# Kernel tuning notes

Measured on AMD Instinct MI355X. Metric: run time of the kernel, lower is better.

## Reference

```python
import jax, jax.numpy as jnp
import numpy as np

B, S, D_IN, E = 64, 199, 1024, 256
INNER, K = 512, 4
NH_M, DH_M = 4, 128
NH_S, DH_S = 4, 64
FF_UP = 384
SLSTM_AT = (1, 4)


def layernorm(x, w, eps=1e-5):
    mu = x.mean(-1, keepdims=True)
    var = x.var(-1, keepdims=True)
    return (x - mu) * jax.lax.rsqrt(var + eps) * w


def mh_layernorm(h, w, eps=1e-5):
    # h: (B,S,NH,DH): normalize per head over DH, scale by w (NH*DH,)
    mu = h.mean(-1, keepdims=True)
    var = h.var(-1, keepdims=True)
    hn = (h - mu) * jax.lax.rsqrt(var + eps)
    b, s, nh, dh = h.shape
    return hn.reshape(b, s, nh * dh) * w


def causal_conv(x, w, b):
    # depthwise causal conv; x (B,S,C), w (C,K), b (C,)
    k = w.shape[-1]
    s = x.shape[1]
    xp = jnp.pad(x, ((0, 0), (k - 1, 0), (0, 0)))
    y = sum(xp[:, i:i + s, :] * w[:, i] for i in range(k))
    return y + b


def headwise(x, w):
    # block-diagonal linear (LinearHeadwiseExpand): x (B,S,H*d), w (H,o,d)
    b, s, _ = x.shape
    h, o, d = w.shape
    y = jnp.einsum('bshd,hod->bsho', x.reshape(b, s, h, d), w)
    return y.reshape(b, s, h * o)


def mlstm_parallel(q, k, v, ig, fg):
    # stabilized parallel mLSTM; q,k,v (B,NH,S,DH); ig,fg (B,NH,S)
    s, dh = q.shape[2], q.shape[3]
    logf = jax.nn.log_sigmoid(fg)
    lfc = jnp.cumsum(logf, axis=-1)
    lfc = jnp.concatenate([jnp.zeros_like(lfc[..., :1]), lfc], axis=-1)  # (B,NH,S+1)
    mat = lfc[..., :, None] - lfc[..., None, :]
    mask = jnp.tril(jnp.ones((s + 1, s + 1), dtype=bool))
    mat = jnp.where(mask, mat, -jnp.inf)
    logD = mat[..., 1:, 1:] + ig[..., None, :]            # (B,NH,S,S)
    maxD = jnp.max(logD, axis=-1, keepdims=True)
    Dm = jnp.exp(logD - maxD)
    qk = jnp.einsum('bnsd,bntd->bnst', q, k) / (dh ** 0.5)
    C = qk * Dm
    norm = jnp.maximum(jnp.abs(C.sum(-1, keepdims=True)), jnp.exp(-maxD))
    return jnp.einsum('bnst,bntd->bnsd', C / (norm + 1e-6), v)


def mlstm_layer(x, proj_up, conv_w, conv_b, q_w, k_w, v_w, ig_w, ig_b, fg_w, fg_b, skip, outnorm_w, proj_down):
    b, s, _ = x.shape
    xi = x @ proj_up                                      # (B,S,2*INNER)
    x_m, z = jnp.split(xi, 2, axis=-1)
    xca = jax.nn.silu(causal_conv(x_m, conv_w, conv_b))
    q = headwise(xca, q_w)
    k = headwise(xca, k_w)
    v = headwise(x_m, v_w)
    gate_in = jnp.concatenate([q, k, v], axis=-1)         # (B,S,3*INNER)
    ig = (gate_in @ ig_w.T + ig_b).transpose(0, 2, 1)     # (B,NH,S)
    fg = (gate_in @ fg_w.T + fg_b).transpose(0, 2, 1)
    qh = q.reshape(b, s, NH_M, DH_M).transpose(0, 2, 1, 3)
    kh = k.reshape(b, s, NH_M, DH_M).transpose(0, 2, 1, 3)
    vh = v.reshape(b, s, NH_M, DH_M).transpose(0, 2, 1, 3)
    h = mlstm_parallel(qh, kh, vh, ig, fg)                # (B,NH,S,DH)
    hn = mh_layernorm(h.transpose(0, 2, 1, 3), outnorm_w) # (B,S,INNER)
    h_state = (hn + skip * xca) * jax.nn.silu(z)
    return h_state @ proj_down


def slstm_layer(x, conv_w, conv_b, gate_w, rec_w, bias, gn_w):
    b, s, _ = x.shape
    xc = jax.nn.silu(causal_conv(x, conv_w, conv_b))
    xch = xc.reshape(b, s, NH_S, DH_S)
    xh = x.reshape(b, s, NH_S, DH_S)
    gi = jnp.einsum('bshd,hod->bsho', xch, gate_w[0])
    gf = jnp.einsum('bshd,hod->bsho', xch, gate_w[1])
    gz = jnp.einsum('bshd,hod->bsho', xh, gate_w[2])
    go = jnp.einsum('bshd,hod->bsho', xh, gate_w[3])
    Wx = jnp.stack([gi, gf, gz, go], axis=2)              # (B,S,4,NH,DH)

    def step(carry, wx):
        h, c, n, m = carry
        raw = wx + jnp.einsum('bhd,ghod->bgho', h, rec_w) + bias
        iraw, fraw, zraw, oraw = raw[:, 0], raw[:, 1], raw[:, 2], raw[:, 3]
        logfplusm = m + jax.nn.log_sigmoid(fraw)
        m_new = jnp.maximum(iraw, logfplusm)
        igate = jnp.exp(iraw - m_new)
        fgate = jnp.exp(logfplusm - m_new)
        c_new = fgate * c + igate * jnp.tanh(zraw)
        n_new = fgate * n + igate
        h_new = jax.nn.sigmoid(oraw) * (c_new / n_new)
        return (h_new, c_new, n_new, m_new), h_new

    z0 = jnp.zeros((b, NH_S, DH_S), x.dtype)
    _, ys = jax.lax.scan(step, (z0, z0, z0, z0), jnp.moveaxis(Wx, 1, 0))
    y = jnp.moveaxis(ys, 0, 1)                            # (B,S,NH,DH)
    return mh_layernorm(y, gn_w)


def gated_ffn(x, w_up, w_dn):
    gate, up = jnp.split(x @ w_up, 2, axis=-1)
    return (jax.nn.gelu(gate) * up) @ w_dn


def forward_fn(x, w_down, b_down, m_ln_w, m_proj_up, m_conv_w, m_conv_b, m_q_w, m_k_w, m_v_w,
               m_ig_w, m_ig_b, m_fg_w, m_fg_b, m_skip, m_outnorm_w, m_proj_down,
               s_ln_w, s_conv_w, s_conv_b, s_gate_w, s_rec_w, s_bias, s_gn_w, s_ln2_w,
               s_ffn_up, s_ffn_down, post_ln_w, w_emo, b_emo, w_sen, b_sen):
    h = x @ w_down + b_down                               # (B,S,E)
    mi = si = 0
    for blk in range(7):
        if blk in SLSTM_AT:
            h = h + slstm_layer(layernorm(h, s_ln_w[si]), s_conv_w[si], s_conv_b[si],
                                s_gate_w[si], s_rec_w[si], s_bias[si], s_gn_w[si])
            h = h + gated_ffn(layernorm(h, s_ln2_w[si]), s_ffn_up[si], s_ffn_down[si])
            si += 1
        else:
            h = h + mlstm_layer(layernorm(h, m_ln_w[mi]), m_proj_up[mi], m_conv_w[mi], m_conv_b[mi],
                                m_q_w[mi], m_k_w[mi], m_v_w[mi], m_ig_w[mi], m_ig_b[mi],
                                m_fg_w[mi], m_fg_b[mi], m_skip[mi], m_outnorm_w[mi], m_proj_down[mi])
            mi += 1
    h = jax.nn.selu(layernorm(h, post_ln_w))
    pooled = h.mean(axis=1)                               # (B,E)
    return pooled @ w_emo + b_emo, pooled @ w_sen + b_sen


def setup_inputs() -> dict:
    ks = iter(jax.random.split(jax.random.key(0), 40))
    def p(*shape, s=0.02):
        return jax.random.normal(next(ks), shape, dtype=jnp.float32) * s
    inp = dict(
        x=jax.random.normal(next(ks), (B, S, D_IN), dtype=jnp.float32),
        w_down=p(D_IN, E), b_down=jnp.zeros((E,), jnp.float32),
        m_ln_w=jnp.ones((5, E), jnp.float32),
        m_proj_up=p(5, E, 2 * INNER),
        m_conv_w=p(5, INNER, K), m_conv_b=jnp.zeros((5, INNER), jnp.float32),
        m_q_w=p(5, 128, 4, 4), m_k_w=p(5, 128, 4, 4), m_v_w=p(5, 128, 4, 4),
        m_ig_w=p(5, NH_M, 3 * INNER), m_ig_b=p(5, NH_M, s=0.1),
        m_fg_w=p(5, NH_M, 3 * INNER),
        m_fg_b=jnp.tile(jnp.linspace(3.0, 6.0, NH_M, dtype=jnp.float32), (5, 1)),
        m_skip=jnp.ones((5, INNER), jnp.float32),
        m_outnorm_w=jnp.ones((5, INNER), jnp.float32),
        m_proj_down=p(5, INNER, E),
        s_ln_w=jnp.ones((2, E), jnp.float32),
        s_conv_w=p(2, E, K), s_conv_b=jnp.zeros((2, E), jnp.float32),
        s_gate_w=p(2, 4, NH_S, DH_S, DH_S),
        s_rec_w=p(2, 4, NH_S, DH_S, DH_S),
        s_bias=jnp.zeros((2, 4, NH_S, DH_S), jnp.float32).at[:, 1].set(3.0),
        s_gn_w=jnp.ones((2, E), jnp.float32),
        s_ln2_w=jnp.ones((2, E), jnp.float32),
        s_ffn_up=p(2, E, 2 * FF_UP), s_ffn_down=p(2, FF_UP, E),
        post_ln_w=jnp.ones((E,), jnp.float32),
        w_emo=p(E, 7), b_emo=jnp.zeros((7,), jnp.float32),
        w_sen=p(E, 3), b_sen=jnp.zeros((3,), jnp.float32),
    )
    return inp


def reference(x, w_down, b_down, m_ln_w, m_proj_up, m_conv_w, m_conv_b, m_q_w, m_k_w, m_v_w,
              m_ig_w, m_ig_b, m_fg_w, m_fg_b, m_skip, m_outnorm_w, m_proj_down,
              s_ln_w, s_conv_w, s_conv_b, s_gate_w, s_rec_w, s_bias, s_gn_w, s_ln2_w,
              s_ffn_up, s_ffn_down, post_ln_w, w_emo, b_emo, w_sen, b_sen):
    return forward_fn(x, w_down, b_down, m_ln_w, m_proj_up, m_conv_w, m_conv_b, m_q_w, m_k_w, m_v_w,
                      m_ig_w, m_ig_b, m_fg_w, m_fg_b, m_skip, m_outnorm_w, m_proj_down,
                      s_ln_w, s_conv_w, s_conv_b, s_gate_w, s_rec_w, s_bias, s_gn_w, s_ln2_w,
                      s_ffn_up, s_ffn_down, post_ln_w, w_emo, b_emo, w_sen, b_sen)
```

## Files before the change

### kernel.cpp

```cpp
#include <hip/hip_runtime.h>
#include <hip/hip_bf16.h>
#include <math.h>


#define B_    64
#define S_    199
#define E_    256
#define NTOK  (B_*S_)
#define NQT   13

typedef __attribute__((ext_vector_type(8))) short short8;
typedef __attribute__((ext_vector_type(4))) float floatx4;
typedef unsigned short ushort_t;

__device__ __forceinline__ float sigmoidf_(float x) { return 1.f / (1.f + expf(-x)); }
__device__ __forceinline__ float siluf_(float x) { return x / (1.f + expf(-x)); }
__device__ __forceinline__ float logsigf_(float x) { return fminf(x, 0.f) - log1pf(expf(-fabsf(x))); }

__device__ __forceinline__ ushort_t f2b(float f) {
    union { float f; unsigned u; } v; v.f = f;
    unsigned r = (v.u + 0x7fffu + ((v.u >> 16) & 1u)) >> 16;
    return (ushort_t)r;
}
__device__ __forceinline__ float bf2f(ushort_t u) {
    union { unsigned u; float f; } v; v.u = ((unsigned)u) << 16;
    return v.f;
}
__device__ __forceinline__ short8 cvt8(const float* p) {
    union { ushort_t us[8]; short8 v; } t;
    #pragma unroll
    for (int i = 0; i < 8; i++) t.us[i] = f2b(p[i]);
    return t.v;
}

__global__ void cvt_bf(const float* __restrict__ in, ushort_t* __restrict__ out, int n4) {
    int i = blockIdx.x * 256 + threadIdx.x;
    if (i >= n4) return;
    float4 v = *(const float4*)&in[i * 4];
    union { ushort_t us[4]; uint2 u; } t;
    t.us[0] = f2b(v.x); t.us[1] = f2b(v.y); t.us[2] = f2b(v.z); t.us[3] = f2b(v.w);
    *(uint2*)&out[i * 4] = t.u;
}

__global__ void __launch_bounds__(256)
gemm_bf(const ushort_t* __restrict__ A, const ushort_t* __restrict__ Bw,
        const float* __restrict__ bias, float* __restrict__ C,
        int M, int K, int N, int accum) {
    __shared__ __align__(16) ushort_t As[64][40];
    __shared__ __align__(16) ushort_t Bs[128][40];
    int tid = threadIdx.x;
    int wave = tid >> 6, lane = tid & 63;
    int wm = wave >> 1, wn = wave & 1;
    int quad = lane >> 4, l16 = lane & 15;
    int m0 = blockIdx.y * 64, n0 = blockIdx.x * 128;
    floatx4 zero = {0.f, 0.f, 0.f, 0.f};
    floatx4 acc[2][4];
    #pragma unroll
    for (int i = 0; i < 2; i++)
        #pragma unroll
        for (int j = 0; j < 4; j++) acc[i][j] = zero;
    int ar = tid >> 2, ac = (tid & 3) * 8;
    int bn = tid & 127, bkg = (tid >> 7) * 16;
    for (int k0 = 0; k0 < K; k0 += 32) {
        *(uint4*)&As[ar][ac] = *(const uint4*)(A + (size_t)(m0 + ar) * K + k0 + ac);
        {
            const ushort_t* bp = Bw + (size_t)(k0 + bkg) * N + n0 + bn;
            union { ushort_t us[16]; uint4 v[2]; } t;
            #pragma unroll
            for (int i = 0; i < 16; i++) t.us[i] = bp[(size_t)i * N];
            *(uint4*)&Bs[bn][bkg] = t.v[0];
            *(uint4*)&Bs[bn][bkg + 8] = t.v[1];
        }
        __syncthreads();
        short8 af[2], bf[4];
        #pragma unroll
        for (int i = 0; i < 2; i++) af[i] = *(const short8*)&As[wm * 32 + i * 16 + l16][quad * 8];
        #pragma unroll
        for (int j = 0; j < 4; j++) bf[j] = *(const short8*)&Bs[wn * 64 + j * 16 + l16][quad * 8];
        #pragma unroll
        for (int i = 0; i < 2; i++)
            #pragma unroll
            for (int j = 0; j < 4; j++)
                acc[i][j] = __builtin_amdgcn_mfma_f32_16x16x32_bf16(af[i], bf[j], acc[i][j], 0, 0, 0);
        __syncthreads();
    }
    #pragma unroll
    for (int i = 0; i < 2; i++)
        #pragma unroll
        for (int j = 0; j < 4; j++)
            #pragma unroll
            for (int r = 0; r < 4; r++) {
                int row = m0 + wm * 32 + i * 16 + quad * 4 + r;
                int col = n0 + wn * 64 + j * 16 + l16;
                float o = acc[i][j][r];
                if (bias) o += bias[col];
                float* cp = &C[(size_t)row * N + col];
                if (accum) o += *cp;
                *cp = o;
            }
}

__global__ void __launch_bounds__(256)
gemm_mfma(const float* __restrict__ A, const float* __restrict__ Bw,
          const float* __restrict__ bias, float* __restrict__ C,
          int M, int K, int N, int accum) {
    __shared__ __align__(16) ushort_t As[64][40];
    __shared__ __align__(16) ushort_t Bs[64][40];
    int tid = threadIdx.x;
    int wave = tid >> 6, lane = tid & 63;
    int wm = wave >> 1, wn = wave & 1;
    int quad = lane >> 4, l16 = lane & 15;
    int m0 = blockIdx.y * 64, n0 = blockIdx.x * 64;
    floatx4 zero = {0.f, 0.f, 0.f, 0.f};
    floatx4 acc[2][2];
    acc[0][0] = zero; acc[0][1] = zero; acc[1][0] = zero; acc[1][1] = zero;
    int ar = tid >> 2, ac = (tid & 3) * 8;
    int bn = tid & 63, bk = (tid >> 6) * 8;
    for (int k0 = 0; k0 < K; k0 += 32) {
        {
            const float* ap = A + (size_t)(m0 + ar) * K + k0 + ac;
            union { ushort_t us[8]; uint4 v; } t;
            #pragma unroll
            for (int i = 0; i < 8; i++) t.us[i] = f2b(ap[i]);
            *(uint4*)&As[ar][ac] = t.v;
        }
        {
            const float* bp = Bw + (size_t)(k0 + bk) * N + n0 + bn;
            union { ushort_t us[8]; uint4 v; } t;
            #pragma unroll
            for (int i = 0; i < 8; i++) t.us[i] = f2b(bp[(size_t)i * N]);
            *(uint4*)&Bs[bn][bk] = t.v;
        }
        __syncthreads();
        short8 af[2], bf[2];
        #pragma unroll
        for (int i = 0; i < 2; i++) af[i] = *(const short8*)&As[wm * 32 + i * 16 + l16][quad * 8];
        #pragma unroll
        for (int j = 0; j < 2; j++) bf[j] = *(const short8*)&Bs[wn * 32 + j * 16 + l16][quad * 8];
        #pragma unroll
        for (int i = 0; i < 2; i++)
            #pragma unroll
            for (int j = 0; j < 2; j++)
                acc[i][j] = __builtin_amdgcn_mfma_f32_16x16x32_bf16(af[i], bf[j], acc[i][j], 0, 0, 0);
        __syncthreads();
    }
    #pragma unroll
    for (int i = 0; i < 2; i++)
        #pragma unroll
        for (int j = 0; j < 2; j++)
            #pragma unroll
            for (int r = 0; r < 4; r++) {
                int row = m0 + wm * 32 + i * 16 + quad * 4 + r;
                int col = n0 + wn * 32 + j * 16 + l16;
                float o = acc[i][j][r];
                if (bias) o += bias[col];
                float* cp = &C[(size_t)row * N + col];
                if (accum) o += *cp;
                *cp = o;
            }
}

__global__ void __launch_bounds__(256)
slstm_wx_mfma(const ushort_t* __restrict__ xc, const ushort_t* __restrict__ xln,
              const float* __restrict__ gw, float* __restrict__ Wx) {
    __shared__ __align__(16) ushort_t As[64][40];
    __shared__ __align__(16) ushort_t Bs[64][40];
    int gh = blockIdx.y; int g = gh >> 2, hh = gh & 3;
    const ushort_t* src = (g < 2) ? xc : xln;
    const float* w = gw + (size_t)gh * 4096;
    int tid = threadIdx.x;
    int wave = tid >> 6, lane = tid & 63;
    int wm = wave >> 1, wn = wave & 1;
    int quad = lane >> 4, l16 = lane & 15;
    int m0 = blockIdx.x * 64;
    floatx4 zero = {0.f, 0.f, 0.f, 0.f};
    floatx4 acc[2][2];
    acc[0][0] = zero; acc[0][1] = zero; acc[1][0] = zero; acc[1][1] = zero;
    int ar = tid >> 2, ac = (tid & 3) * 8;
    int bn = tid & 63, bk = (tid >> 6) * 8;
    #pragma unroll
    for (int kt = 0; kt < 2; kt++) {
        int k0 = kt * 32;
        *(uint4*)&As[ar][ac] = *(const uint4*)(src + (size_t)(m0 + ar) * 256 + hh * 64 + k0 + ac);
        {
            const float* bp = w + (size_t)bn * 64 + k0 + bk;
            union { ushort_t us[8]; uint4 v; } t;
            #pragma unroll
            for (int i = 0; i < 8; i++) t.us[i] = f2b(bp[i]);
            *(uint4*)&Bs[bn][bk] = t.v;
        }
        __syncthreads();
        short8 af[2], bf[2];
        #pragma unroll
        for (int i = 0; i < 2; i++) af[i] = *(const short8*)&As[wm * 32 + i * 16 + l16][quad * 8];
        #pragma unroll
        for (int j = 0; j < 2; j++) bf[j] = *(const short8*)&Bs[wn * 32 + j * 16 + l16][quad * 8];
        #pragma unroll
        for (int i = 0; i < 2; i++)
            #pragma unroll
            for (int j = 0; j < 2; j++)
                acc[i][j] = __builtin_amdgcn_mfma_f32_16x16x32_bf16(af[i], bf[j], acc[i][j], 0, 0, 0);
        __syncthreads();
    }
    #pragma unroll
    for (int i = 0; i < 2; i++)
        #pragma unroll
        for (int j = 0; j < 2; j++)
            #pragma unroll
            for (int r = 0; r < 4; r++) {
                int row = m0 + wm * 32 + i * 16 + quad * 4 + r;
                int col = wn * 32 + j * 16 + l16;
                Wx[(size_t)row * 1024 + g * 256 + hh * 64 + col] = acc[i][j][r];
            }
}

__global__ void __launch_bounds__(256)
layernorm256(const float* __restrict__ x, const float* __restrict__ w, ushort_t* __restrict__ y) {
    int n = blockIdx.x, t = threadIdx.x;
    float v = x[(size_t)n * 256 + t];
    float s = v, s2 = v * v;
    #pragma unroll
    for (int off = 32; off; off >>= 1) { s += __shfl_xor(s, off); s2 += __shfl_xor(s2, off); }
    __shared__ float ps[4], ps2[4];
    if ((t & 63) == 0) { ps[t >> 6] = s; ps2[t >> 6] = s2; }
    __syncthreads();
    float S = ps[0] + ps[1] + ps[2] + ps[3];
    float S2 = ps2[0] + ps2[1] + ps2[2] + ps2[3];
    float mu = S / 256.f, var = S2 / 256.f - mu * mu;
    y[(size_t)n * 256 + t] = f2b((v - mu) * rsqrtf(var + 1e-5f) * w[t]);
}

__global__ void __launch_bounds__(256)
postln_selu(const float* __restrict__ x, const float* __restrict__ w, float* __restrict__ y) {
    int n = blockIdx.x, t = threadIdx.x;
    float v = x[(size_t)n * 256 + t];
    float s = v, s2 = v * v;
    #pragma unroll
    for (int off = 32; off; off >>= 1) { s += __shfl_xor(s, off); s2 += __shfl_xor(s2, off); }
    __shared__ float ps[4], ps2[4];
    if ((t & 63) == 0) { ps[t >> 6] = s; ps2[t >> 6] = s2; }
    __syncthreads();
    float S = ps[0] + ps[1] + ps[2] + ps[3];
    float S2 = ps2[0] + ps2[1] + ps2[2] + ps2[3];
    float mu = S / 256.f, var = S2 / 256.f - mu * mu;
    float yn = (v - mu) * rsqrtf(var + 1e-5f) * w[t];
    y[(size_t)n * 256 + t] = 1.0507009873554805f * (yn > 0.f ? yn : 1.6732632423543772f * (expf(yn) - 1.f));
}

__global__ void conv_silu_m(const float* __restrict__ xi, const float* __restrict__ cw,
                            const float* __restrict__ cb, float* __restrict__ xca) {
    int idx = blockIdx.x * blockDim.x + threadIdx.x;
    if (idx >= NTOK * 512) return;
    int n = idx >> 9, c = idx & 511;
    int b = n / S_, s = n - b * S_;
    float y = cb[c];
    #pragma unroll
    for (int i = 0; i < 4; i++) {
        int sp = s - 3 + i;
        if (sp >= 0) y += xi[(size_t)(b * S_ + sp) * 1024 + c] * cw[c * 4 + i];
    }
    xca[idx] = siluf_(y);
}

__global__ void headwise_qkv(const float* __restrict__ xca, const float* __restrict__ xi,
                             const float* __restrict__ qw, const float* __restrict__ kw,
                             const float* __restrict__ vw,
                             float* __restrict__ qb, float* __restrict__ kb, float* __restrict__ vb) {
    int idx = blockIdx.x * blockDim.x + threadIdx.x;
    if (idx >= NTOK * 512) return;
    int n = idx >> 9, c = idx & 511;
    int hh = c >> 2, o = c & 3;
    float aq = 0, ak = 0, av = 0;
    #pragma unroll
    for (int d = 0; d < 4; d++) {
        float xc = xca[(size_t)n * 512 + hh * 4 + d];
        float xm = xi[(size_t)n * 1024 + hh * 4 + d];
        int wi = (hh * 4 + o) * 4 + d;
        aq += xc * qw[wi]; ak += xc * kw[wi]; av += xm * vw[wi];
    }
    qb[idx] = aq; kb[idx] = ak; vb[idx] = av;
}

__global__ void __launch_bounds__(256)
mlstm_gates(const float* __restrict__ qb, const float* __restrict__ kb, const float* __restrict__ vb,
            const float* __restrict__ igw, const float* __restrict__ igbias,
            const float* __restrict__ fgw, const float* __restrict__ fgbias,
            float* __restrict__ igo, float* __restrict__ fgo) {
    int gid = blockIdx.x * 256 + threadIdx.x;
    int wid = gid >> 6, lane = gid & 63;
    int which = wid & 1, hd = (wid >> 1) & 3, n = wid >> 3;
    if (n >= NTOK) return;
    const float* w = (which ? fgw : igw) + hd * 1536;
    float a = 0.f;
    for (int j = lane; j < 512; j += 64) {
        a += qb[(size_t)n * 512 + j] * w[j]
           + kb[(size_t)n * 512 + j] * w[512 + j]
           + vb[(size_t)n * 512 + j] * w[1024 + j];
    }
    #pragma unroll
    for (int off = 32; off; off >>= 1) a += __shfl_xor(a, off);
    if (lane == 0) {
        a += (which ? fgbias : igbias)[hd];
        (which ? fgo : igo)[(size_t)n * 4 + hd] = a;
    }
}

__global__ void __launch_bounds__(256)
mlstm_cumsum(const float* __restrict__ fgo, const float* __restrict__ igo,
             float* __restrict__ lfc, float* __restrict__ Mx) {
    int bh = blockIdx.x * 4 + (threadIdx.x >> 6);
    int lane = threadIdx.x & 63;
    int b = bh >> 2, h = bh & 3;
    float v[4]; float lsum = 0.f;
    #pragma unroll
    for (int i = 0; i < 4; i++) {
        int s = lane * 4 + i;
        float f = (s < S_) ? fgo[(size_t)(b * S_ + s) * 4 + h] : 0.f;
        lsum += logsigf_(f);
        v[i] = lsum;
    }
    float x = lsum;
    #pragma unroll
    for (int off = 1; off < 64; off <<= 1) {
        float y = __shfl_up(x, off);
        if (lane >= off) x += y;
    }
    float excl = x - lsum;
    float lf1[4];
    #pragma unroll
    for (int i = 0; i < 4; i++) lf1[i] = excl + v[i];
    if (lane == 0) lfc[bh * (S_ + 1)] = 0.f;
    #pragma unroll
    for (int i = 0; i < 4; i++) {
        int s = lane * 4 + i;
        if (s < S_) lfc[bh * (S_ + 1) + s + 1] = lf1[i];
    }
    float gm[4]; float lmax = -1e30f;
    #pragma unroll
    for (int i = 0; i < 4; i++) {
        int s = lane * 4 + i;
        float ig_ = (s < S_) ? igo[(size_t)(b * S_ + s) * 4 + h] : -1e30f;
        float gg = ig_ - lf1[i];
        lmax = fmaxf(lmax, gg);
        gm[i] = lmax;
    }
    float xm = lmax;
    #pragma unroll
    for (int off = 1; off < 64; off <<= 1) {
        float y = __shfl_up(xm, off);
        if (lane >= off) xm = fmaxf(xm, y);
    }
    float exclm = __shfl_up(xm, 1);
    if (lane == 0) exclm = -1e30f;
    #pragma unroll
    for (int i = 0; i < 4; i++) {
        int s = lane * 4 + i;
        if (s < S_) Mx[bh * S_ + s] = fmaxf(exclm, gm[i]);
    }
}

__global__ void __launch_bounds__(256, 1)
mlstm_attn_mfma(const float* __restrict__ qb, const float* __restrict__ kb, const float* __restrict__ vb,
                const float* __restrict__ igb, const float* __restrict__ lfc, const float* __restrict__ Mx,
                float* __restrict__ outb) {
    __shared__ __align__(16) ushort_t Kb[64 * 136];
    __shared__ __align__(16) ushort_t Vt[128 * 72];
    __shared__ __align__(16) ushort_t Pw[4][16 * 72];
    __shared__ float gv[208], lfv[208], mxv[208];
    int bh = blockIdx.x; int b = bh >> 2, h = bh & 3;
    int tid = threadIdx.x, wave = tid >> 6, lane = tid & 63;
    int quad = lane >> 4, l16 = lane & 15;
    if (tid < 208) {
        if (tid < S_) {
            float lf1 = lfc[bh * (S_ + 1) + tid + 1];
            gv[tid] = igb[(size_t)(b * S_ + tid) * 4 + h] - lf1;
            lfv[tid] = lf1;
            mxv[tid] = Mx[bh * S_ + tid];
        } else { gv[tid] = 0.f; lfv[tid] = 0.f; mxv[tid] = 0.f; }
    }
    floatx4 zero = {0.f, 0.f, 0.f, 0.f};
    float rs[4][4];
    floatx4 accv[4][8];
    #pragma unroll
    for (int qi = 0; qi < 4; qi++) {
        #pragma unroll
        for (int r = 0; r < 4; r++) rs[qi][r] = 0.f;
        #pragma unroll
        for (int dt = 0; dt < 8; dt++) accv[qi][dt] = zero;
    }
    const float scale = 0.08838834764831845f;
    int trow = tid >> 4, d0 = (tid & 15) * 8;
    for (int c = 0; c < 4; c++) {
        __syncthreads();
        #pragma unroll
        for (int i = 0; i < 4; i++) {
            int tl = trow + 16 * i;
            int t = c * 64 + tl;
            union { ushort_t us[8]; uint4 v; } kk;
            ushort_t vv[8];
            if (t < S_) {
                const float* kp = kb + (size_t)(b * S_ + t) * 512 + h * 128 + d0;
                const float* vp = vb + (size_t)(b * S_ + t) * 512 + h * 128 + d0;
                #pragma unroll
                for (int ii = 0; ii < 8; ii++) { kk.us[ii] = f2b(kp[ii]); vv[ii] = f2b(vp[ii]); }
            } else {
                kk.v = (uint4){0, 0, 0, 0};
                #pragma unroll
                for (int ii = 0; ii < 8; ii++) vv[ii] = 0;
            }
            *(uint4*)&Kb[tl * 136 + d0] = kk.v;
            #pragma unroll
            for (int ii = 0; ii < 8; ii++) Vt[(d0 + ii) * 72 + tl] = vv[ii];
        }
        __syncthreads();
        for (int qi = 0; qi < 4; qi++) {
            int qt = wave + 4 * qi;
            if (qt >= NQT || qt < 4 * c) continue;
            uint4 z4 = {0, 0, 0, 0};
            for (int z = lane; z < 144; z += 64) ((uint4*)Pw[wave])[z] = z4;
            int srow = qt * 16 + l16;
            const float* qp = qb + (size_t)(b * S_ + min(srow, S_ - 1)) * 512 + h * 128 + quad * 8;
            short8 af[4];
            #pragma unroll
            for (int ks = 0; ks < 4; ks++) af[ks] = cvt8(qp + 32 * ks);
            int ktmax_l = min(qt, 4 * c + 3) - 4 * c;
            for (int ktl = 0; ktl <= ktmax_l; ktl++) {
                floatx4 acc = zero;
                #pragma unroll
                for (int ks = 0; ks < 4; ks++) {
                    short8 bf = *(const short8*)&Kb[(ktl * 16 + l16) * 136 + quad * 8 + 32 * ks];
                    acc = __builtin_amdgcn_mfma_f32_16x16x32_bf16(af[ks], bf, acc, 0, 0, 0);
                }
                int tcol = c * 64 + ktl * 16 + l16;
                float gt = gv[tcol];
                #pragma unroll
                for (int r = 0; r < 4; r++) {
                    int s = qt * 16 + quad * 4 + r;
                    bool valid = (tcol <= s) && (tcol < S_);
                    float w = valid ? expf(gt - mxv[s]) : 0.f;
                    float p = acc[r] * scale * w;
                    rs[qi][r] += p;
                    Pw[wave][(quad * 4 + r) * 72 + ktl * 16 + l16] = f2b(p);
                }
            }
            #pragma unroll
            for (int dt = 0; dt < 8; dt++) {
                floatx4 a = accv[qi][dt];
                #pragma unroll
                for (int ks = 0; ks < 2; ks++) {
                    short8 ap = *(const short8*)&Pw[wave][l16 * 72 + quad * 8 + 32 * ks];
                    short8 bp = *(const short8*)&Vt[(dt * 16 + l16) * 72 + quad * 8 + 32 * ks];
                    a = __builtin_amdgcn_mfma_f32_16x16x32_bf16(ap, bp, a, 0, 0, 0);
                }
                accv[qi][dt] = a;
            }
        }
    }
    for (int qi = 0; qi < 4; qi++) {
        int qt = wave + 4 * qi;
        if (qt >= NQT) continue;
        float nrm[4];
        #pragma unroll
        for (int r = 0; r < 4; r++) {
            float v = rs[qi][r];
            v += __shfl_xor(v, 1); v += __shfl_xor(v, 2);
            v += __shfl_xor(v, 4); v += __shfl_xor(v, 8);
            int s = qt * 16 + quad * 4 + r;
            nrm[r] = fmaxf(fabsf(v), expf(-(lfv[s] + mxv[s]))) + 1e-6f;
        }
        #pragma unroll
        for (int dt = 0; dt < 8; dt++)
            #pragma unroll
            for (int r = 0; r < 4; r++) {
                int s = qt * 16 + quad * 4 + r;
                if (s < S_)
                    outb[(size_t)(b * S_ + s) * 512 + h * 128 + dt * 16 + l16] = accv[qi][dt][r] / nrm[r];
            }
    }
}

__global__ void __launch_bounds__(512)
mhln_m(float* __restrict__ hatt, const float* __restrict__ w) {
    int n = blockIdx.x, t = threadIdx.x;
    float v = hatt[(size_t)n * 512 + t];
    float s = v, s2 = v * v;
    #pragma unroll
    for (int off = 32; off; off >>= 1) { s += __shfl_xor(s, off); s2 += __shfl_xor(s2, off); }
    __shared__ float ps[8], ps2[8];
    if ((t & 63) == 0) { ps[t >> 6] = s; ps2[t >> 6] = s2; }
    __syncthreads();
    int hd = t >> 7;
    float S = ps[hd * 2] + ps[hd * 2 + 1], S2 = ps2[hd * 2] + ps2[hd * 2 + 1];
    float mu = S / 128.f, var = S2 / 128.f - mu * mu;
    hatt[(size_t)n * 512 + t] = (v - mu) * rsqrtf(var + 1e-5f) * w[t];
}

__global__ void hstate_m(const float* __restrict__ hatt, const float* __restrict__ xca,
                         const float* __restrict__ xi, const float* __restrict__ skip,
                         ushort_t* __restrict__ out16) {
    int idx = blockIdx.x * blockDim.x + threadIdx.x;
    if (idx >= NTOK * 512) return;
    int n = idx >> 9, c = idx & 511;
    float z = xi[(size_t)n * 1024 + 512 + c];
    out16[idx] = f2b((hatt[idx] + skip[c] * xca[idx]) * siluf_(z));
}

__global__ void conv_silu_s(const ushort_t* __restrict__ xln, const float* __restrict__ cw,
                            const float* __restrict__ cb, ushort_t* __restrict__ xc) {
    int idx = blockIdx.x * blockDim.x + threadIdx.x;
    if (idx >= NTOK * 256) return;
    int n = idx >> 8, c = idx & 255;
    int b = n / S_, s = n - b * S_;
    float y = cb[c];
    #pragma unroll
    for (int i = 0; i < 4; i++) {
        int sp = s - 3 + i;
        if (sp >= 0) y += bf2f(xln[(size_t)(b * S_ + sp) * 256 + c]) * cw[c * 4 + i];
    }
    xc[idx] = f2b(siluf_(y));
}

__global__ void __launch_bounds__(512)
slstm_rec(const float* __restrict__ Wx, const float* __restrict__ rw,
          const float* __restrict__ bias, float* __restrict__ ys) {
    int b = blockIdx.x >> 2, h = blockIdx.x & 3;
    int tid = threadIdx.x;
    int g = tid >> 7;
    int o = (tid >> 1) & 63;
    int kh = tid & 1;
    float w[32];
    const float* wp = rw + (size_t)(((g * 4 + h) * 64 + o)) * 64 + kh * 32;
    #pragma unroll
    for (int d = 0; d < 32; d++) w[d] = wp[d];
    float bi = bias[(g * 4 + h) * 64 + o];
    __shared__ __align__(16) float hs[64];
    __shared__ float raws[4][64];
    if (tid < 64) hs[tid] = 0.f;
    float c_ = 0.f, n_ = 0.f, m_ = 0.f;
    size_t wxbase = (size_t)(b * S_) * 1024 + g * 256 + h * 64 + o;
    float wx_cur = Wx[wxbase];
    __syncthreads();
    for (int s = 0; s < S_; s++) {
        float wx_next = (s + 1 < S_) ? Wx[wxbase + (size_t)(s + 1) * 1024] : 0.f;
        float a0 = 0.f, a1 = 0.f, a2 = 0.f, a3 = 0.f;
        const float* hb = hs + kh * 32;
        #pragma unroll
        for (int d4 = 0; d4 < 8; d4++) {
            float4 hv = *(const float4*)&hb[d4 * 4];
            a0 += hv.x * w[4 * d4 + 0];
            a1 += hv.y * w[4 * d4 + 1];
            a2 += hv.z * w[4 * d4 + 2];
            a3 += hv.w * w[4 * d4 + 3];
        }
        float a = (a0 + a1) + (a2 + a3);
        a += __shfl_xor(a, 1);
        if (kh == 0) raws[g][o] = a + wx_cur + bi;
        __syncthreads();
        float ir = raws[0][o], fr = raws[1][o], zr = raws[2][o], orr = raws[3][o];
        float lfpm = m_ + logsigf_(fr);
        float mn = fmaxf(ir, lfpm);
        float ig = expf(ir - mn), fg = expf(lfpm - mn);
        c_ = fg * c_ + ig * tanhf(zr);
        n_ = fg * n_ + ig;
        m_ = mn;
        float hn = sigmoidf_(orr) * (c_ / n_);
        if (g == 0 && kh == 0) {
            hs[o] = hn;
            ys[(size_t)(b * S_ + s) * 256 + h * 64 + o] = hn;
        }
        __syncthreads();
        wx_cur = wx_next;
    }
}

__global__ void __launch_bounds__(256)
mhln_s_resid(const float* __restrict__ ys, const float* __restrict__ w, float* __restrict__ h) {
    int n = blockIdx.x, t = threadIdx.x;
    float v = ys[(size_t)n * 256 + t];
    float s = v, s2 = v * v;
    #pragma unroll
    for (int off = 32; off; off >>= 1) { s += __shfl_xor(s, off); s2 += __shfl_xor(s2, off); }
    float mu = s / 64.f, var = s2 / 64.f - mu * mu;
    h[(size_t)n * 256 + t] += (v - mu) * rsqrtf(var + 1e-5f) * w[t];
}

__global__ void ffn_act(const float* __restrict__ up, ushort_t* __restrict__ act) {
    int idx = blockIdx.x * blockDim.x + threadIdx.x;
    if (idx >= NTOK * 384) return;
    int n = idx / 384, j = idx - n * 384;
    float g = up[(size_t)n * 768 + j], u = up[(size_t)n * 768 + 384 + j];
    float t = tanhf(0.7978845608028654f * (g + 0.044715f * g * g * g));
    act[idx] = f2b(0.5f * g * (1.f + t) * u);
}

__global__ void pool_k(const float* __restrict__ a, float* __restrict__ pooled) {
    int b = blockIdx.x, e = threadIdx.x;
    float s = 0.f;
    for (int t = 0; t < S_; t++) s += a[(size_t)(b * S_ + t) * 256 + e];
    pooled[b * 256 + e] = s / (float)S_;
}

__global__ void heads_k(const float* __restrict__ pooled,
                        const float* __restrict__ we, const float* __restrict__ be,
                        const float* __restrict__ ws, const float* __restrict__ bs,
                        float* __restrict__ out) {
    int i = blockIdx.x * blockDim.x + threadIdx.x;
    if (i < B_ * 7) {
        int b = i / 7, o = i - b * 7;
        float a = be[o];
        for (int e = 0; e < 256; e++) a += pooled[b * 256 + e] * we[e * 7 + o];
        out[b * 7 + o] = a;
    } else if (i < B_ * 7 + B_ * 3) {
        int j = i - B_ * 7;
        int b = j / 3, o = j - b * 3;
        float a = bs[o];
        for (int e = 0; e < 256; e++) a += pooled[b * 256 + e] * ws[e * 3 + o];
        out[B_ * 7 + b * 3 + o] = a;
    }
}

extern "C" void kernel_launch(void* const* d_in, const int* in_sizes, int n_in,
                              void* d_out, int out_size, void* d_ws, size_t ws_size,
                              hipStream_t stream) {
    (void)in_sizes; (void)n_in; (void)out_size; (void)ws_size;
    const float* x          = (const float*)d_in[0];
    const float* w_down     = (const float*)d_in[1];
    const float* b_down     = (const float*)d_in[2];
    const float* m_ln_w     = (const float*)d_in[3];
    const float* m_proj_up  = (const float*)d_in[4];
    const float* m_conv_w   = (const float*)d_in[5];
    const float* m_conv_b   = (const float*)d_in[6];
    const float* m_q_w      = (const float*)d_in[7];
    const float* m_k_w      = (const float*)d_in[8];
    const float* m_v_w      = (const float*)d_in[9];
    const float* m_ig_w     = (const float*)d_in[10];
    const float* m_ig_b     = (const float*)d_in[11];
    const float* m_fg_w     = (const float*)d_in[12];
    const float* m_fg_b     = (const float*)d_in[13];
    const float* m_skip     = (const float*)d_in[14];
    const float* m_outnorm  = (const float*)d_in[15];
    const float* m_proj_dn  = (const float*)d_in[16];
    const float* s_ln_w     = (const float*)d_in[17];
    const float* s_conv_w   = (const float*)d_in[18];
    const float* s_conv_b   = (const float*)d_in[19];
    const float* s_gate_w   = (const float*)d_in[20];
    const float* s_rec_w    = (const float*)d_in[21];
    const float* s_bias     = (const float*)d_in[22];
    const float* s_gn_w     = (const float*)d_in[23];
    const float* s_ln2_w    = (const float*)d_in[24];
    const float* s_ffn_up   = (const float*)d_in[25];
    const float* s_ffn_dn   = (const float*)d_in[26];
    const float* post_ln_w  = (const float*)d_in[27];
    const float* w_emo      = (const float*)d_in[28];
    const float* b_emo      = (const float*)d_in[29];
    const float* w_sen      = (const float*)d_in[30];
    const float* b_sen      = (const float*)d_in[31];

    float* W    = (float*)d_ws;
    float* h    = W;
    float* lnb  = h    + (size_t)NTOK * 256;
    float* big0 = lnb  + (size_t)NTOK * 256;
    float* xca  = big0 + (size_t)NTOK * 1024;
    float* qb   = xca  + (size_t)NTOK * 512;
    float* kb   = qb   + (size_t)NTOK * 512;
    float* vb   = kb   + (size_t)NTOK * 512;
    float* hatt = vb   + (size_t)NTOK * 512;
    float* igo  = hatt + (size_t)NTOK * 512;
    float* fgo  = igo  + (size_t)NTOK * 4;
    float* lfcb = fgo  + (size_t)NTOK * 4;
    float* Mxb  = lfcb + (size_t)256 * (S_ + 1);
    float* pooled = Mxb + (size_t)256 * S_;
    ushort_t* lnb16 = (ushort_t*)lnb;
    ushort_t* hat16 = (ushort_t*)kb;
    ushort_t* xc16  = (ushort_t*)vb;
    ushort_t* wpk   = (ushort_t*)(pooled + 64 * 256);
    ushort_t* wp_pu = wpk;
    ushort_t* wp_pd = wp_pu + 5 * 262144;
    ushort_t* wp_fu = wp_pd + 5 * 131072;
    ushort_t* wp_fd = wp_fu + 2 * 196608;

    cvt_bf<<<(5 * 262144 / 4 + 255) / 256, 256, 0, stream>>>(m_proj_up, wp_pu, 5 * 262144 / 4);
    cvt_bf<<<(5 * 131072 / 4 + 255) / 256, 256, 0, stream>>>(m_proj_dn, wp_pd, 5 * 131072 / 4);
    cvt_bf<<<(2 * 196608 / 4 + 255) / 256, 256, 0, stream>>>(s_ffn_up, wp_fu, 2 * 196608 / 4);
    cvt_bf<<<(2 * 98304 / 4 + 255) / 256, 256, 0, stream>>>(s_ffn_dn, wp_fd, 2 * 98304 / 4);

    gemm_mfma<<<dim3(256 / 64, NTOK / 64), 256, 0, stream>>>(x, w_down, b_down, h, NTOK, 1024, 256, 0);

    int mi = 0, si = 0;
    for (int blk = 0; blk < 7; blk++) {
        if (blk == 1 || blk == 4) {
            layernorm256<<<NTOK, 256, 0, stream>>>(h, s_ln_w + si * 256, lnb16);
            conv_silu_s<<<(NTOK * 256 + 255) / 256, 256, 0, stream>>>(lnb16, s_conv_w + si * 1024, s_conv_b + si * 256, xc16);
            slstm_wx_mfma<<<dim3(NTOK / 64, 16), 256, 0, stream>>>(xc16, lnb16, s_gate_w + (size_t)si * 65536, big0);
            slstm_rec<<<256, 512, 0, stream>>>(big0, s_rec_w + (size_t)si * 65536, s_bias + si * 1024, hatt);
            mhln_s_resid<<<NTOK, 256, 0, stream>>>(hatt, s_gn_w + si * 256, h);
            layernorm256<<<NTOK, 256, 0, stream>>>(h, s_ln2_w + si * 256, lnb16);
            gemm_bf<<<dim3(768 / 128, NTOK / 64), 256, 0, stream>>>(lnb16, wp_fu + (size_t)si * 196608, nullptr, big0, NTOK, 256, 768, 0);
            ffn_act<<<(NTOK * 384 + 255) / 256, 256, 0, stream>>>(big0, hat16);
            gemm_bf<<<dim3(256 / 128, NTOK / 64), 256, 0, stream>>>(hat16, wp_fd + (size_t)si * 98304, nullptr, h, NTOK, 384, 256, 1);
            si++;
        } else {
            layernorm256<<<NTOK, 256, 0, stream>>>(h, m_ln_w + mi * 256, lnb16);
            gemm_bf<<<dim3(1024 / 128, NTOK / 64), 256, 0, stream>>>(lnb16, wp_pu + (size_t)mi * 262144, nullptr, big0, NTOK, 256, 1024, 0);
            conv_silu_m<<<(NTOK * 512 + 255) / 256, 256, 0, stream>>>(big0, m_conv_w + mi * 2048, m_conv_b + mi * 512, xca);
            headwise_qkv<<<(NTOK * 512 + 255) / 256, 256, 0, stream>>>(xca, big0, m_q_w + mi * 2048, m_k_w + mi * 2048, m_v_w + mi * 2048, qb, kb, vb);
            mlstm_gates<<<NTOK * 2, 256, 0, stream>>>(qb, kb, vb, m_ig_w + mi * 6144, m_ig_b + mi * 4, m_fg_w + mi * 6144, m_fg_b + mi * 4, igo, fgo);
            mlstm_cumsum<<<64, 256, 0, stream>>>(fgo, igo, lfcb, Mxb);
            mlstm_attn_mfma<<<256, 256, 0, stream>>>(qb, kb, vb, igo, lfcb, Mxb, hatt);
            mhln_m<<<NTOK, 512, 0, stream>>>(hatt, m_outnorm + mi * 512);
            hstate_m<<<(NTOK * 512 + 255) / 256, 256, 0, stream>>>(hatt, xca, big0, m_skip + mi * 512, hat16);
            gemm_bf<<<dim3(256 / 128, NTOK / 64), 256, 0, stream>>>(hat16, wp_pd + (size_t)mi * 131072, nullptr, h, NTOK, 512, 256, 1);
            mi++;
        }
    }

    postln_selu<<<NTOK, 256, 0, stream>>>(h, post_ln_w, xca);
    pool_k<<<B_, 256, 0, stream>>>(xca, pooled);
    heads_k<<<3, 256, 0, stream>>>(pooled, w_emo, b_emo, w_sen, b_sen, (float*)d_out);
}
```

Before: 2.289 ms.

## Fuse mLSTM conv/qkv, store q/k/v in bf16, fuse out-norm with hstate

Merges the causal conv+SiLU and headwise q/k/v projections into one kernel that writes q/k/v as bf16. The gate projection is rewritten to read the bf16 tensors, with one wave per token computing all eight gate dot products. The attention kernel now loads bf16 directly instead of converting fp32 on the fly. The multi-head layernorm is fused with the h-state/skip/gating kernel. The sLSTM recurrent weights move from registers to shared memory. These changes cut launches and global memory traffic, at the cost of bf16 rounding for the gate inputs and extra LDS pressure in the recurrence.

```diff
diff --git a/kernel.cpp b/kernel.cpp
--- a/kernel.cpp
+++ b/kernel.cpp
@@ -26,11 +26,10 @@
     union { unsigned u; float f; } v; v.u = ((unsigned)u) << 16;
     return v.f;
 }
-__device__ __forceinline__ short8 cvt8(const float* p) {
-    union { ushort_t us[8]; short8 v; } t;
-    #pragma unroll
-    for (int i = 0; i < 8; i++) t.us[i] = f2b(p[i]);
-    return t.v;
+__device__ __forceinline__ void unp2(unsigned d, float& lo, float& hi) {
+    union { unsigned u; float f; } a, b;
+    a.u = d << 16; b.u = d & 0xffff0000u;
+    lo = a.f; hi = b.f;
 }
 
 __global__ void cvt_bf(const float* __restrict__ in, ushort_t* __restrict__ out, int n4) {
@@ -247,61 +246,100 @@
     y[(size_t)n * 256 + t] = 1.0507009873554805f * (yn > 0.f ? yn : 1.6732632423543772f * (expf(yn) - 1.f));
 }
 
-__global__ void conv_silu_m(const float* __restrict__ xi, const float* __restrict__ cw,
-                            const float* __restrict__ cb, float* __restrict__ xca) {
-    int idx = blockIdx.x * blockDim.x + threadIdx.x;
-    if (idx >= NTOK * 512) return;
-    int n = idx >> 9, c = idx & 511;
+__global__ void __launch_bounds__(256)
+fused_qkv(const float* __restrict__ xi, const float* __restrict__ cw,
+          const float* __restrict__ cb,
+          const float* __restrict__ qw, const float* __restrict__ kw,
+          const float* __restrict__ vw,
+          float* __restrict__ xca,
+          ushort_t* __restrict__ q16, ushort_t* __restrict__ k16, ushort_t* __restrict__ v16) {
+    int idx = blockIdx.x * 256 + threadIdx.x;
+    if (idx >= NTOK * 128) return;
+    int n = idx >> 7, hh = idx & 127;
     int b = n / S_, s = n - b * S_;
-    float y = cb[c];
+    int c0 = hh * 4;
+    float4 hist[4];
     #pragma unroll
     for (int i = 0; i < 4; i++) {
         int sp = s - 3 + i;
-        if (sp >= 0) y += xi[(size_t)(b * S_ + sp) * 1024 + c] * cw[c * 4 + i];
-    }
-    xca[idx] = siluf_(y);
-}
-
-__global__ void headwise_qkv(const float* __restrict__ xca, const float* __restrict__ xi,
-                             const float* __restrict__ qw, const float* __restrict__ kw,
-                             const float* __restrict__ vw,
-                             float* __restrict__ qb, float* __restrict__ kb, float* __restrict__ vb) {
-    int idx = blockIdx.x * blockDim.x + threadIdx.x;
-    if (idx >= NTOK * 512) return;
-    int n = idx >> 9, c = idx & 511;
-    int hh = c >> 2, o = c & 3;
-    float aq = 0, ak = 0, av = 0;
+        if (sp >= 0) hist[i] = *(const float4*)(xi + (size_t)(b * S_ + sp) * 1024 + c0);
+        else hist[i] = (float4){0.f, 0.f, 0.f, 0.f};
+    }
+    float xm[4] = {hist[3].x, hist[3].y, hist[3].z, hist[3].w};
+    float xc4[4];
     #pragma unroll
     for (int d = 0; d < 4; d++) {
-        float xc = xca[(size_t)n * 512 + hh * 4 + d];
-        float xm = xi[(size_t)n * 1024 + hh * 4 + d];
-        int wi = (hh * 4 + o) * 4 + d;
-        aq += xc * qw[wi]; ak += xc * kw[wi]; av += xm * vw[wi];
-    }
-    qb[idx] = aq; kb[idx] = ak; vb[idx] = av;
-}
-
-__global__ void __launch_bounds__(256)
-mlstm_gates(const float* __restrict__ qb, const float* __restrict__ kb, const float* __restrict__ vb,
-            const float* __restrict__ igw, const float* __restrict__ igbias,
-            const float* __restrict__ fgw, const float* __restrict__ fgbias,
-            float* __restrict__ igo, float* __restrict__ fgo) {
-    int gid = blockIdx.x * 256 + threadIdx.x;
-    int wid = gid >> 6, lane = gid & 63;
-    int which = wid & 1, hd = (wid >> 1) & 3, n = wid >> 3;
-    if (n >= NTOK) return;
-    const float* w = (which ? fgw : igw) + hd * 1536;
-    float a = 0.f;
-    for (int j = lane; j < 512; j += 64) {
-        a += qb[(size_t)n * 512 + j] * w[j]
-           + kb[(size_t)n * 512 + j] * w[512 + j]
-           + vb[(size_t)n * 512 + j] * w[1024 + j];
-    }
-    #pragma unroll
-    for (int off = 32; off; off >>= 1) a += __shfl_xor(a, off);
-    if (lane == 0) {
-        a += (which ? fgbias : igbias)[hd];
-        (which ? fgo : igo)[(size_t)n * 4 + hd] = a;
+        float y = cb[c0 + d];
+        const float* cwp = cw + (c0 + d) * 4;
+        y += hist[0].x * 0.f;
+        float hv[4] = { d==0?hist[0].x:(d==1?hist[0].y:(d==2?hist[0].z:hist[0].w)),
+                        d==0?hist[1].x:(d==1?hist[1].y:(d==2?hist[1].z:hist[1].w)),
+                        d==0?hist[2].x:(d==1?hist[2].y:(d==2?hist[2].z:hist[2].w)),
+                        xm[d] };
+        #pragma unroll
+        for (int i = 0; i < 4; i++) y += hv[i] * cwp[i];
+        xc4[d] = siluf_(y);
+    }
+    *(float4*)(xca + (size_t)n * 512 + c0) = (float4){xc4[0], xc4[1], xc4[2], xc4[3]};
+    union { ushort_t us[4]; uint2 u; } qo, ko, vo;
+    #pragma unroll
+    for (int o = 0; o < 4; o++) {
+        const float* qp = qw + (c0 + o) * 4;
+        const float* kp = kw + (c0 + o) * 4;
+        const float* vp = vw + (c0 + o) * 4;
+        float aq = 0.f, ak = 0.f, av = 0.f;
+        #pragma unroll
+        for (int d = 0; d < 4; d++) {
+            aq += xc4[d] * qp[d];
+            ak += xc4[d] * kp[d];
+            av += xm[d] * vp[d];
+        }
+        qo.us[o] = f2b(aq); ko.us[o] = f2b(ak); vo.us[o] = f2b(av);
+    }
+    *(uint2*)(q16 + (size_t)n * 512 + c0) = qo.u;
+    *(uint2*)(k16 + (size_t)n * 512 + c0) = ko.u;
+    *(uint2*)(v16 + (size_t)n * 512 + c0) = vo.u;
+}
+
+__global__ void __launch_bounds__(256)
+gates2(const ushort_t* __restrict__ qb, const ushort_t* __restrict__ kb, const ushort_t* __restrict__ vb,
+       const float* __restrict__ igw, const float* __restrict__ igbias,
+       const float* __restrict__ fgw, const float* __restrict__ fgbias,
+       float* __restrict__ igo, float* __restrict__ fgo) {
+    int n = blockIdx.x * 4 + (threadIdx.x >> 6);
+    int lane = threadIdx.x & 63;
+    uint4 q4 = *(const uint4*)(qb + (size_t)n * 512 + lane * 8);
+    uint4 k4 = *(const uint4*)(kb + (size_t)n * 512 + lane * 8);
+    uint4 v4 = *(const uint4*)(vb + (size_t)n * 512 + lane * 8);
+    float q[8], k[8], v[8];
+    unp2(q4.x, q[0], q[1]); unp2(q4.y, q[2], q[3]); unp2(q4.z, q[4], q[5]); unp2(q4.w, q[6], q[7]);
+    unp2(k4.x, k[0], k[1]); unp2(k4.y, k[2], k[3]); unp2(k4.z, k[4], k[5]); unp2(k4.w, k[6], k[7]);
+    unp2(v4.x, v[0], v[1]); unp2(v4.y, v[2], v[3]); unp2(v4.z, v[4], v[5]); unp2(v4.w, v[6], v[7]);
+    float acc[8];
+    #pragma unroll
+    for (int hd = 0; hd < 4; hd++)
+        #pragma unroll
+        for (int wh = 0; wh < 2; wh++) {
+            const float* w = (wh ? fgw : igw) + hd * 1536 + lane * 8;
+            float a = 0.f;
+            #pragma unroll
+            for (int i = 0; i < 8; i++) a += q[i] * w[i];
+            #pragma unroll
+            for (int i = 0; i < 8; i++) a += k[i] * w[512 + i];
+            #pragma unroll
+            for (int i = 0; i < 8; i++) a += v[i] * w[1024 + i];
+            acc[hd * 2 + wh] = a;
+        }
+    #pragma unroll
+    for (int t = 0; t < 8; t++) {
+        float a = acc[t];
+        #pragma unroll
+        for (int off = 32; off; off >>= 1) a += __shfl_xor(a, off);
+        if (lane == 0) {
+            int hd = t >> 1, wh = t & 1;
+            a += (wh ? fgbias : igbias)[hd];
+            (wh ? fgo : igo)[(size_t)n * 4 + hd] = a;
+        }
     }
 }
 
@@ -360,7 +398,7 @@
 }
 
 __global__ void __launch_bounds__(256, 1)
-mlstm_attn_mfma(const float* __restrict__ qb, const float* __restrict__ kb, const float* __restrict__ vb,
+mlstm_attn_mfma(const ushort_t* __restrict__ qb, const ushort_t* __restrict__ kb, const ushort_t* __restrict__ vb,
                 const float* __restrict__ igb, const float* __restrict__ lfc, const float* __restrict__ Mx,
                 float* __restrict__ outb) {
     __shared__ __align__(16) ushort_t Kb[64 * 136];
@@ -396,21 +434,17 @@
         for (int i = 0; i < 4; i++) {
             int tl = trow + 16 * i;
             int t = c * 64 + tl;
-            union { ushort_t us[8]; uint4 v; } kk;
-            ushort_t vv[8];
+            union { ushort_t us[8]; uint4 v; } kk, vv;
             if (t < S_) {
-                const float* kp = kb + (size_t)(b * S_ + t) * 512 + h * 128 + d0;
-                const float* vp = vb + (size_t)(b * S_ + t) * 512 + h * 128 + d0;
-                #pragma unroll
-                for (int ii = 0; ii < 8; ii++) { kk.us[ii] = f2b(kp[ii]); vv[ii] = f2b(vp[ii]); }
+                kk.v = *(const uint4*)(kb + (size_t)(b * S_ + t) * 512 + h * 128 + d0);
+                vv.v = *(const uint4*)(vb + (size_t)(b * S_ + t) * 512 + h * 128 + d0);
             } else {
                 kk.v = (uint4){0, 0, 0, 0};
-                #pragma unroll
-                for (int ii = 0; ii < 8; ii++) vv[ii] = 0;
+                vv.v = (uint4){0, 0, 0, 0};
             }
             *(uint4*)&Kb[tl * 136 + d0] = kk.v;
             #pragma unroll
-            for (int ii = 0; ii < 8; ii++) Vt[(d0 + ii) * 72 + tl] = vv[ii];
+            for (int ii = 0; ii < 8; ii++) Vt[(d0 + ii) * 72 + tl] = vv.us[ii];
         }
         __syncthreads();
         for (int qi = 0; qi < 4; qi++) {
@@ -419,10 +453,10 @@
             uint4 z4 = {0, 0, 0, 0};
             for (int z = lane; z < 144; z += 64) ((uint4*)Pw[wave])[z] = z4;
             int srow = qt * 16 + l16;
-            const float* qp = qb + (size_t)(b * S_ + min(srow, S_ - 1)) * 512 + h * 128 + quad * 8;
+            const ushort_t* qp = qb + (size_t)(b * S_ + min(srow, S_ - 1)) * 512 + h * 128 + quad * 8;
             short8 af[4];
             #pragma unroll
-            for (int ks = 0; ks < 4; ks++) af[ks] = cvt8(qp + 32 * ks);
+            for (int ks = 0; ks < 4; ks++) af[ks] = *(const short8*)(qp + 32 * ks);
             int ktmax_l = min(qt, 4 * c + 3) - 4 * c;
             for (int ktl = 0; ktl <= ktmax_l; ktl++) {
                 floatx4 acc = zero;
@@ -480,7 +514,9 @@
 }
 
 __global__ void __launch_bounds__(512)
-mhln_m(float* __restrict__ hatt, const float* __restrict__ w) {
+mhln_hstate(const float* __restrict__ hatt, const float* __restrict__ w,
+            const float* __restrict__ xca, const float* __restrict__ xi,
+            const float* __restrict__ skip, ushort_t* __restrict__ out16) {
     int n = blockIdx.x, t = threadIdx.x;
     float v = hatt[(size_t)n * 512 + t];
     float s = v, s2 = v * v;
@@ -492,17 +528,9 @@
     int hd = t >> 7;
     float S = ps[hd * 2] + ps[hd * 2 + 1], S2 = ps2[hd * 2] + ps2[hd * 2 + 1];
     float mu = S / 128.f, var = S2 / 128.f - mu * mu;
-    hatt[(size_t)n * 512 + t] = (v - mu) * rsqrtf(var + 1e-5f) * w[t];
-}
-
-__global__ void hstate_m(const float* __restrict__ hatt, const float* __restrict__ xca,
-                         const float* __restrict__ xi, const float* __restrict__ skip,
-                         ushort_t* __restrict__ out16) {
-    int idx = blockIdx.x * blockDim.x + threadIdx.x;
-    if (idx >= NTOK * 512) return;
-    int n = idx >> 9, c = idx & 511;
-    float z = xi[(size_t)n * 1024 + 512 + c];
-    out16[idx] = f2b((hatt[idx] + skip[c] * xca[idx]) * siluf_(z));
+    float hn = (v - mu) * rsqrtf(var + 1e-5f) * w[t];
+    float z = xi[(size_t)n * 1024 + 512 + t];
+    out16[(size_t)n * 512 + t] = f2b((hn + skip[t] * xca[(size_t)n * 512 + t]) * siluf_(z));
 }
 
 __global__ void conv_silu_s(const ushort_t* __restrict__ xln, const float* __restrict__ cw,
@@ -523,18 +551,17 @@
 __global__ void __launch_bounds__(512)
 slstm_rec(const float* __restrict__ Wx, const float* __restrict__ rw,
           const float* __restrict__ bias, float* __restrict__ ys) {
+    __shared__ __align__(16) float wl[512 * 36];
+    __shared__ __align__(16) float hs[64];
+    __shared__ float raws[4][64];
     int b = blockIdx.x >> 2, h = blockIdx.x & 3;
     int tid = threadIdx.x;
-    int g = tid >> 7;
-    int o = (tid >> 1) & 63;
-    int kh = tid & 1;
-    float w[32];
+    int g = tid >> 7, o = (tid >> 1) & 63, kh = tid & 1;
     const float* wp = rw + (size_t)(((g * 4 + h) * 64 + o)) * 64 + kh * 32;
-    #pragma unroll
-    for (int d = 0; d < 32; d++) w[d] = wp[d];
+    float* myrow = wl + tid * 36;
+    #pragma unroll
+    for (int i = 0; i < 8; i++) *(float4*)&myrow[i * 4] = *(const float4*)&wp[i * 4];
     float bi = bias[(g * 4 + h) * 64 + o];
-    __shared__ __align__(16) float hs[64];
-    __shared__ float raws[4][64];
     if (tid < 64) hs[tid] = 0.f;
     float c_ = 0.f, n_ = 0.f, m_ = 0.f;
     size_t wxbase = (size_t)(b * S_) * 1024 + g * 256 + h * 64 + o;
@@ -543,14 +570,14 @@
     for (int s = 0; s < S_; s++) {
         float wx_next = (s + 1 < S_) ? Wx[wxbase + (size_t)(s + 1) * 1024] : 0.f;
         float a0 = 0.f, a1 = 0.f, a2 = 0.f, a3 = 0.f;
-        const float* hb = hs + kh * 32;
         #pragma unroll
         for (int d4 = 0; d4 < 8; d4++) {
-            float4 hv = *(const float4*)&hb[d4 * 4];
-            a0 += hv.x * w[4 * d4 + 0];
-            a1 += hv.y * w[4 * d4 + 1];
-            a2 += hv.z * w[4 * d4 + 2];
-            a3 += hv.w * w[4 * d4 + 3];
+            float4 wv = *(const float4*)&myrow[d4 * 4];
+            float4 hv = *(const float4*)&hs[kh * 32 + d4 * 4];
+            a0 += hv.x * wv.x;
+            a1 += hv.y * wv.y;
+            a2 += hv.z * wv.z;
+            a3 += hv.w * wv.w;
         }
         float a = (a0 + a1) + (a2 + a3);
         a += __shfl_xor(a, 1);
@@ -671,8 +698,11 @@
     float* Mxb  = lfcb + (size_t)256 * (S_ + 1);
     float* pooled = Mxb + (size_t)256 * S_;
     ushort_t* lnb16 = (ushort_t*)lnb;
-    ushort_t* hat16 = (ushort_t*)kb;
-    ushort_t* xc16  = (ushort_t*)vb;
+    ushort_t* qb16  = (ushort_t*)qb;
+    ushort_t* kb16  = (ushort_t*)kb;
+    ushort_t* vb16  = (ushort_t*)vb;
+    ushort_t* hat16 = qb16 + (size_t)NTOK * 512;
+    ushort_t* xc16  = (ushort_t*)(vb16 + (size_t)NTOK * 512);
     ushort_t* wpk   = (ushort_t*)(pooled + 64 * 256);
     ushort_t* wp_pu = wpk;
     ushort_t* wp_pd = wp_pu + 5 * 262144;
@@ -702,13 +732,14 @@
         } else {
             layernorm256<<<NTOK, 256, 0, stream>>>(h, m_ln_w + mi * 256, lnb16);
             gemm_bf<<<dim3(1024 / 128, NTOK / 64), 256, 0, stream>>>(lnb16, wp_pu + (size_t)mi * 262144, nullptr, big0, NTOK, 256, 1024, 0);
-            conv_silu_m<<<(NTOK * 512 + 255) / 256, 256, 0, stream>>>(big0, m_conv_w + mi * 2048, m_conv_b + mi * 512, xca);
-            headwise_qkv<<<(NTOK * 512 + 255) / 256, 256, 0, stream>>>(xca, big0, m_q_w + mi * 2048, m_k_w + mi * 2048, m_v_w + mi * 2048, qb, kb, vb);
-            mlstm_gates<<<NTOK * 2, 256, 0, stream>>>(qb, kb, vb, m_ig_w + mi * 6144, m_ig_b + mi * 4, m_fg_w + mi * 6144, m_fg_b + mi * 4, igo, fgo);
+            fused_qkv<<<(NTOK * 128 + 255) / 256, 256, 0, stream>>>(big0, m_conv_w + mi * 2048, m_conv_b + mi * 512,
+                                                                    m_q_w + mi * 2048, m_k_w + mi * 2048, m_v_w + mi * 2048,
+                                                                    xca, qb16, kb16, vb16);
+            gates2<<<NTOK / 4, 256, 0, stream>>>(qb16, kb16, vb16, m_ig_w + mi * 6144, m_ig_b + mi * 4,
+                                                 m_fg_w + mi * 6144, m_fg_b + mi * 4, igo, fgo);
             mlstm_cumsum<<<64, 256, 0, stream>>>(fgo, igo, lfcb, Mxb);
-            mlstm_attn_mfma<<<256, 256, 0, stream>>>(qb, kb, vb, igo, lfcb, Mxb, hatt);
-            mhln_m<<<NTOK, 512, 0, stream>>>(hatt, m_outnorm + mi * 512);
-            hstate_m<<<(NTOK * 512 + 255) / 256, 256, 0, stream>>>(hatt, xca, big0, m_skip + mi * 512, hat16);
+            mlstm_attn_mfma<<<256, 256, 0, stream>>>(qb16, kb16, vb16, igo, lfcb, Mxb, hatt);
+            mhln_hstate<<<NTOK, 512, 0, stream>>>(hatt, m_outnorm + mi * 512, xca, big0, m_skip + mi * 512, hat16);
             gemm_bf<<<dim3(256 / 128, NTOK / 64), 256, 0, stream>>>(hat16, wp_pd + (size_t)mi * 131072, nullptr, h, NTOK, 512, 256, 1);
             mi++;
         }
```

Measured after the change: 1.989 ms. 1.15x faster.
